# Kernel optimization log

Measured on AMD Instinct MI355X. Metric: run time of the kernel, lower is better.

The kernel has to match this reference:

```python
import jax, jax.numpy as jnp
import numpy as np

B, N, E, D, H, OUT = 4, 20000, 320000, 64, 128, 64
EPS = 1e-5


def layernorm(x, g, b):
    m = x.mean(-1, keepdims=True)
    v = x.var(-1, keepdims=True)
    return (x - m) / jnp.sqrt(v + EPS) * g + b


def setup_inputs() -> dict:
    key = jax.random.key(0)
    ks = jax.random.split(key, 20)
    nodes = jax.random.normal(ks[0], (B, N, D), jnp.float32)
    edges = jax.random.randint(ks[1], (B, E, 2), 0, N)
    edge_weights = jax.random.uniform(ks[2], (B, E), dtype=jnp.float32)
    s = 0.05
    inp = {"nodes": nodes, "edges": edges, "edge_weights": edge_weights}
    dims = [(3 * D, H), (H, H), (H, H), (H, OUT)]
    for i, (di, do) in enumerate(dims, start=1):
        inp[f"W{i}"] = jax.random.normal(ks[2 + 4 * i], (di, do), jnp.float32) * s
        inp[f"b{i}"] = jax.random.normal(ks[3 + 4 * i], (do,), jnp.float32) * s
        inp[f"g{i}"] = 1.0 + jax.random.normal(ks[4 + 4 * i], (do,), jnp.float32) * s
        inp[f"t{i}"] = jax.random.normal(ks[5 + 4 * i], (do,), jnp.float32) * s
    return inp


def reference(nodes, edges, edge_weights,
              W1, b1, g1, t1, W2, b2, g2, t2,
              W3, b3, g3, t3, W4, b4, g4, t4):
    # gather source/dest node features per edge: [B, E, D]
    src_idx = edges[..., 0]  # [B, E]
    dst_idx = edges[..., 1]  # [B, E]
    w = edge_weights[..., None]  # [B, E, 1]
    in_feat = jnp.take_along_axis(nodes, src_idx[..., None], axis=1) * w
    out_feat = jnp.take_along_axis(nodes, dst_idx[..., None], axis=1) * w

    # scatter-sum per node (segment sum over flattened batch*node ids)
    off = jnp.arange(B, dtype=dst_idx.dtype)[:, None] * N
    agg_in = jax.ops.segment_sum(in_feat.reshape(B * E, D),
                                 (dst_idx + off).reshape(-1),
                                 num_segments=B * N).reshape(B, N, D)
    agg_out = jax.ops.segment_sum(out_feat.reshape(B * E, D),
                                  (src_idx + off).reshape(-1),
                                  num_segments=B * N).reshape(B, N, D)

    x = jnp.concatenate([agg_in, agg_out, nodes], axis=2)  # [B, N, 3D]
    x = jnp.tanh(layernorm(x @ W1 + b1, g1, t1))
    x = jnp.tanh(layernorm(x @ W2 + b2, g2, t2))
    x = jnp.tanh(layernorm(x @ W3 + b3, g3, t3))
    x = jnp.tanh(layernorm(x @ W4 + b4, g4, t4))
    return x
```

## Files before the change

### kernel.cpp

```cpp
#include <hip/hip_runtime.h>
#include <math.h>

constexpr int Bc   = 4;
constexpr int Nc   = 20000;
constexpr int Ec   = 320000;
constexpr int Dc   = 64;
constexpr int ROWS = Bc * Nc;
constexpr int NSL  = 79;
constexpr int NBK  = 2 * Bc * NSL;
constexpr int CAP  = 48;
constexpr int EPW  = 2560;
constexpr int WPB  = 125;
constexpr int NWG  = Bc * WPB;
constexpr int TPW  = 128;
#define EPS 1e-5f

typedef __attribute__((ext_vector_type(8))) _Float16 f16x8;
typedef __attribute__((ext_vector_type(4))) float f32x4;

constexpr int CH32  = 5120;
constexpr int CH4c  = 2560;
constexpr int WQ_L2 = 30720;
constexpr int WQ_L3 = 51200;
constexpr int WQ_L4 = 71680;
constexpr int WQ_TOT = 81920;

__global__ __launch_bounds__(256) void conv_nodes(
    const float* __restrict__ nodes, _Float16* __restrict__ n16) {
    int i = (blockIdx.x * 256 + threadIdx.x) * 8;
    float4 a = *(const float4*)(nodes + i);
    float4 b = *(const float4*)(nodes + i + 4);
    f16x8 h;
    h[0] = (_Float16)a.x; h[1] = (_Float16)a.y; h[2] = (_Float16)a.z; h[3] = (_Float16)a.w;
    h[4] = (_Float16)b.x; h[5] = (_Float16)b.y; h[6] = (_Float16)b.z; h[7] = (_Float16)b.w;
    *(f16x8*)(n16 + i) = h;
}

__global__ __launch_bounds__(256) void local_bin(
    const int2* __restrict__ edges, const float* __restrict__ ew,
    uint2* __restrict__ staging, int* __restrict__ tblS, int* __restrict__ tblC) {
    __shared__ int cnt[256];
    __shared__ int offs[256];
    __shared__ int wsum[4];
    __shared__ uint2 stg[EPW * 2];

    const int tid = threadIdx.x;
    const int wg  = blockIdx.x;
    const int b   = wg / WPB;
    const int wgl = wg - b * WPB;
    const int base = wg * EPW;
    const int lane = tid & 63, wid = tid >> 6;

    cnt[tid] = 0;
    __syncthreads();

    int2 e[10]; unsigned wb[10];
#pragma unroll
    for (int j = 0; j < 10; ++j) {
        int idx = base + j * 256 + tid;
        e[j]  = edges[idx];
        wb[j] = __float_as_uint(ew[idx]);
    }

#pragma unroll
    for (int j = 0; j < 10; ++j) {
        atomicAdd(&cnt[e[j].y >> 8], 1);
        atomicAdd(&cnt[79 + (e[j].x >> 8)], 1);
    }
    __syncthreads();

    int v = cnt[tid];
    int incl = v;
#pragma unroll
    for (int d = 1; d < 64; d <<= 1) {
        int t = __shfl_up(incl, d, 64);
        if (lane >= d) incl += t;
    }
    if (lane == 63) wsum[wid] = incl;
    __syncthreads();
    int add = 0;
#pragma unroll
    for (int w = 0; w < 4; ++w)
        if (w < wid) add += wsum[w];
    offs[tid] = incl - v + add;
    __syncthreads();

    if (tid < 158) {
        int lb = tid;
        int row = (lb < 79) ? (b * NSL + lb) : (Bc * NSL + b * NSL + (lb - 79));
        tblS[row * TPW + wgl] = offs[lb];
        tblC[row * TPW + wgl] = cnt[lb];
    }
    __syncthreads();

#pragma unroll
    for (int j = 0; j < 10; ++j) {
        int pA = atomicAdd(&offs[e[j].y >> 8], 1);
        stg[pA] = make_uint2(((unsigned)(e[j].y & 255) << 16) | (unsigned)e[j].x, wb[j]);
        int pB = atomicAdd(&offs[79 + (e[j].x >> 8)], 1);
        stg[pB] = make_uint2(((unsigned)(e[j].x & 255) << 16) | (unsigned)e[j].y, wb[j]);
    }
    __syncthreads();

    uint2* outp = staging + (size_t)wg * (EPW * 2);
#pragma unroll
    for (int it = 0; it < 20; ++it)
        outp[it * 256 + tid] = stg[it * 256 + tid];
}

__global__ __launch_bounds__(512) void sort_bins(
    const uint2* __restrict__ staging,
    const int* __restrict__ tblS, const int* __restrict__ tblC,
    unsigned* __restrict__ list, int* __restrict__ cnt) {
    __shared__ unsigned lds[256 * CAP];
    __shared__ int lcnt[256];
    __shared__ int segS[WPB], segC[WPB];

    const int tid    = threadIdx.x;
    const int bucket = blockIdx.x;
    const int lane   = tid & 63, wid = tid >> 6;

    const int dir   = bucket >= Bc * NSL;
    const int rem   = bucket - dir * Bc * NSL;
    const int b     = rem / NSL;
    const int slice = rem % NSL;
    const int node0 = slice << 8;

    for (int i = tid; i < 256 * CAP; i += 512) lds[i] = 0u;
    if (tid < 256) lcnt[tid] = 0;
    if (tid < WPB) {
        int st = tblS[bucket * TPW + tid];
        int c  = tblC[bucket * TPW + tid];
        if (st < 0) st = 0; if (st > EPW * 2) st = EPW * 2;
        if (c  < 0) c  = 0; if (c  > EPW * 2 - st) c = EPW * 2 - st;
        segS[tid] = st;
        segC[tid] = c;
    }
    __syncthreads();

    for (int s = wid; s < WPB; s += 8) {
        int c = segC[s];
        const uint2* sp = staging + (size_t)(b * WPB + s) * (EPW * 2) + segS[s];
        for (int l0 = 0; l0 < c; l0 += 64) {
            if (lane < c - l0) {
                uint2 en = sp[l0 + lane];
                int local = en.x >> 16;
                unsigned nbr  = en.x & 0xFFFFu;
                unsigned wtop = (en.y + 0x4000u) & 0xFFFF8000u;
                int p = atomicAdd(&lcnt[local], 1);
                if (p < CAP) lds[local * CAP + p] = wtop | nbr;
            }
        }
    }
    __syncthreads();

    int nvalid = Nc - node0; if (nvalid > 256) nvalid = 256;
    const int keybase = dir * ROWS + b * Nc + node0;

    if (tid < nvalid) {
        int vv = lcnt[tid];
        cnt[keybase + tid] = vv < CAP ? vv : CAP;
    }
    unsigned* outp = list + (size_t)keybase * CAP;
    const int total = nvalid * CAP;
    for (int i = tid; i < total; i += 512)
        outp[i] = lds[i];
}

__global__ __launch_bounds__(256) void gather_kernel(
    const _Float16* __restrict__ n16,
    const unsigned* __restrict__ list,
    const int* __restrict__ cnt,
    _Float16* __restrict__ agg16_in, _Float16* __restrict__ agg16_out) {
    const int wid  = __builtin_amdgcn_readfirstlane(threadIdx.x >> 6);
    const int lane = threadIdx.x & 63;
    const int bid  = blockIdx.x;
    const int xcd  = bid & 7;
    const int loc  = bid >> 3;
    const int key  = xcd * 20000 + loc * 4 + wid;
    const int dir  = key >= ROWS;
    const int bn   = key - dir * ROWS;
    const int b    = bn / Nc;
    const _Float16* nb = n16 + (size_t)b * Nc * Dc;

    const int c = cnt[key];
    const unsigned* lp = list + (size_t)key * CAP;
    float acc0 = 0.f, acc1 = 0.f;
    for (int i = 0; i < c; i += 16) {
        uint4 ea = *(const uint4*)(lp + i);
        uint4 eb = *(const uint4*)(lp + i + 4);
        uint4 ec = *(const uint4*)(lp + i + 8);
        uint4 ed = *(const uint4*)(lp + i + 12);
        unsigned ev[16] = {ea.x, ea.y, ea.z, ea.w, eb.x, eb.y, eb.z, eb.w,
                           ec.x, ec.y, ec.z, ec.w, ed.x, ed.y, ed.z, ed.w};
        unsigned se[16];
        float r[16];
#pragma unroll
        for (int j = 0; j < 16; ++j) {
            se[j] = __builtin_amdgcn_readfirstlane(ev[j]);
            const _Float16* rp = nb + ((size_t)(se[j] & 0x7FFFu) << 6);
            r[j] = (float)rp[lane];
        }
#pragma unroll
        for (int j = 0; j < 16; j += 2) {
            acc0 = fmaf(r[j],     __uint_as_float(se[j]     & 0xFFFF8000u), acc0);
            acc1 = fmaf(r[j + 1], __uint_as_float(se[j + 1] & 0xFFFF8000u), acc1);
        }
    }
    float acc = acc0 + acc1;
    _Float16* dst = dir ? agg16_out : agg16_in;
    dst[(size_t)bn * Dc + lane] = (_Float16)acc;
}

__device__ inline float fast_tanh(float x) {
    float e = exp2f(x * 2.885390081777927f);
    return 1.0f - 2.0f * __builtin_amdgcn_rcpf(e + 1.0f);
}

__global__ __launch_bounds__(256) void prep_w(
    const float* __restrict__ W1, const float* __restrict__ W2,
    const float* __restrict__ W3, const float* __restrict__ W4,
    _Float16* __restrict__ wp) {
    int idx = blockIdx.x * 256 + threadIdx.x;
    const float* W; int DOl, base;
    if (idx < WQ_L2)      { W = W1; DOl = 128; base = 0; }
    else if (idx < WQ_L3) { W = W2; DOl = 128; base = WQ_L2; }
    else if (idx < WQ_L4) { W = W3; DOl = 128; base = WQ_L3; }
    else                  { W = W4; DOl = 64;  base = WQ_L4; }
    int local = idx - base;
    int chsz = DOl * 40;
    int chunk = local / chsz, rem = local - chunk * chsz;
    int col = rem / 40, kk = rem - col * 40;
    int k = chunk * 32 + kk;
    float v = (kk < 32) ? W[(size_t)k * DOl + col] : 0.f;
    wp[idx] = (_Float16)v;
}

__global__ __launch_bounds__(256, 4) void mlp_fused(
    const _Float16* __restrict__ agg16_in,
    const _Float16* __restrict__ agg16_out,
    const _Float16* __restrict__ n16,
    const _Float16* __restrict__ wp,
    const float* __restrict__ b1, const float* __restrict__ g1, const float* __restrict__ t1,
    const float* __restrict__ b2, const float* __restrict__ g2, const float* __restrict__ t2,
    const float* __restrict__ b3, const float* __restrict__ g3, const float* __restrict__ t3,
    const float* __restrict__ b4, const float* __restrict__ g4, const float* __restrict__ t4,
    float* __restrict__ out) {
    constexpr int XS = 136;
    __shared__ __align__(16) _Float16 wbuf[2][CH32];
    __shared__ __align__(16) _Float16 xh[64 * XS];

    const int tid = threadIdx.x;
    const int wv  = tid >> 6;
    const int l   = tid & 63;
    const int lm  = l & 15;
    const int lg  = l >> 4;
    const int rowloc = wv * 16;
    const int arow = blockIdx.x * 64 + rowloc + lm;
    const int koff = lg * 8;

    uint4 s0_ = {}, s1_ = {}, s2_ = {};

#define STAGE_LOAD(OFFH, N4)                                                      \
    {                                                                             \
        const uint4* s_ = (const uint4*)(wp + (OFFH));                            \
        if (tid < (N4))       s0_ = s_[tid];                                      \
        if (tid + 256 < (N4)) s1_ = s_[tid + 256];                                \
        if (tid + 512 < (N4)) s2_ = s_[tid + 512];                                \
    }
#define STAGE_WRITE(BUFI, N4)                                                     \
    {                                                                             \
        uint4* d_ = (uint4*)wbuf[BUFI];                                           \
        if (tid < (N4))       d_[tid] = s0_;                                      \
        if (tid + 256 < (N4)) d_[tid + 256] = s1_;                                \
        if (tid + 512 < (N4)) d_[tid + 512] = s2_;                                \
    }

    f32x4 acc[8] = {};
#define ZERO_ACC                                                                  \
    {                                                                             \
        _Pragma("unroll")                                                         \
        for (int ct = 0; ct < 8; ++ct) acc[ct] = (f32x4){0.f, 0.f, 0.f, 0.f};     \
    }

#define L1_COMPUTE(BUFI, SRC16, SUBK)                                             \
    {                                                                             \
        f16x8 ah = *(const f16x8*)((SRC16) + (size_t)arow * 64 + (SUBK) * 32 + koff); \
        _Pragma("unroll")                                                         \
        for (int ct = 0; ct < 8; ++ct) {                                          \
            int col = ct * 16 + lm;                                               \
            f16x8 bh = *(const f16x8*)(wbuf[BUFI] + col * 40 + koff);             \
            acc[ct] = __builtin_amdgcn_mfma_f32_16x16x32_f16(ah, bh, acc[ct], 0, 0, 0); \
        }                                                                         \
    }

#define LX_COMPUTE(BUFI, KIDX, NCTv)                                              \
    {                                                                             \
        f16x8 ah = *(const f16x8*)(xh + (rowloc + lm) * XS + (KIDX) * 32 + koff); \
        _Pragma("unroll")                                                         \
        for (int ct = 0; ct < NCTv; ++ct) {                                       \
            int col = ct * 16 + lm;                                               \
            f16x8 bh = *(const f16x8*)(wbuf[BUFI] + col * 40 + koff);             \
            acc[ct] = __builtin_amdgcn_mfma_f32_16x16x32_f16(ah, bh, acc[ct], 0, 0, 0); \
        }                                                                         \
    }

#define EPILOGUE(NCTv, DOv, BIAS, GG, TT, STORE_LDS)                              \
    {                                                                             \
        float s[4] = {0, 0, 0, 0}, ss[4] = {0, 0, 0, 0};                          \
        _Pragma("unroll")                                                         \
        for (int ct = 0; ct < NCTv; ++ct) {                                       \
            float bc = BIAS[ct * 16 + lm];                                        \
            _Pragma("unroll")                                                     \
            for (int r = 0; r < 4; ++r) {                                         \
                float v = acc[ct][r] + bc;                                        \
                acc[ct][r] = v;                                                   \
                s[r] += v; ss[r] += v * v;                                        \
            }                                                                     \
        }                                                                         \
        _Pragma("unroll")                                                         \
        for (int m = 1; m < 16; m <<= 1) {                                        \
            _Pragma("unroll")                                                     \
            for (int r = 0; r < 4; ++r) {                                         \
                s[r]  += __shfl_xor(s[r],  m, 64);                                \
                ss[r] += __shfl_xor(ss[r], m, 64);                                \
            }                                                                     \
        }                                                                         \
        float mean[4], rstd[4];                                                   \
        _Pragma("unroll")                                                         \
        for (int r = 0; r < 4; ++r) {                                             \
            mean[r] = s[r] * (1.0f / DOv);                                        \
            float var = ss[r] * (1.0f / DOv) - mean[r] * mean[r];                 \
            rstd[r] = rsqrtf(var + EPS);                                          \
        }                                                                         \
        _Pragma("unroll")                                                         \
        for (int ct = 0; ct < NCTv; ++ct) {                                       \
            int col = ct * 16 + lm;                                               \
            float gc = GG[col], tc = TT[col];                                     \
            _Pragma("unroll")                                                     \
            for (int r = 0; r < 4; ++r) {                                         \
                float v = (acc[ct][r] - mean[r]) * rstd[r] * gc + tc;             \
                float th = fast_tanh(v);                                          \
                int row = rowloc + lg * 4 + r;                                    \
                if (STORE_LDS) {                                                  \
                    xh[row * XS + col] = (_Float16)th;                            \
                } else {                                                          \
                    out[(size_t)(blockIdx.x * 64 + row) * 64 + col] = th;         \
                }                                                                 \
            }                                                                     \
        }                                                                         \
    }

    STAGE_LOAD(0, 640)
    STAGE_WRITE(0, 640)
    __syncthreads();

    STAGE_LOAD(CH32, 640)
    L1_COMPUTE(0, agg16_in, 0)
    STAGE_WRITE(1, 640)
    __syncthreads();

    STAGE_LOAD(2 * CH32, 640)
    L1_COMPUTE(1, agg16_in, 1)
    STAGE_WRITE(0, 640)
    __syncthreads();

    STAGE_LOAD(3 * CH32, 640)
    L1_COMPUTE(0, agg16_out, 0)
    STAGE_WRITE(1, 640)
    __syncthreads();

    STAGE_LOAD(4 * CH32, 640)
    L1_COMPUTE(1, agg16_out, 1)
    STAGE_WRITE(0, 640)
    __syncthreads();

    STAGE_LOAD(5 * CH32, 640)
    L1_COMPUTE(0, n16, 0)
    STAGE_WRITE(1, 640)
    __syncthreads();

    STAGE_LOAD(WQ_L2, 640)
    L1_COMPUTE(1, n16, 1)
    EPILOGUE(8, 128, b1, g1, t1, 1)
    STAGE_WRITE(0, 640)
    __syncthreads();
    ZERO_ACC

    STAGE_LOAD(WQ_L2 + CH32, 640)
    LX_COMPUTE(0, 0, 8)
    STAGE_WRITE(1, 640)
    __syncthreads();

    STAGE_LOAD(WQ_L2 + 2 * CH32, 640)
    LX_COMPUTE(1, 1, 8)
    STAGE_WRITE(0, 640)
    __syncthreads();

    STAGE_LOAD(WQ_L2 + 3 * CH32, 640)
    LX_COMPUTE(0, 2, 8)
    STAGE_WRITE(1, 640)
    __syncthreads();

    STAGE_LOAD(WQ_L3, 640)
    LX_COMPUTE(1, 3, 8)
    EPILOGUE(8, 128, b2, g2, t2, 1)
    STAGE_WRITE(0, 640)
    __syncthreads();
    ZERO_ACC

    STAGE_LOAD(WQ_L3 + CH32, 640)
    LX_COMPUTE(0, 0, 8)
    STAGE_WRITE(1, 640)
    __syncthreads();

    STAGE_LOAD(WQ_L3 + 2 * CH32, 640)
    LX_COMPUTE(1, 1, 8)
    STAGE_WRITE(0, 640)
    __syncthreads();

    STAGE_LOAD(WQ_L3 + 3 * CH32, 640)
    LX_COMPUTE(0, 2, 8)
    STAGE_WRITE(1, 640)
    __syncthreads();

    STAGE_LOAD(WQ_L4, 320)
    LX_COMPUTE(1, 3, 8)
    EPILOGUE(8, 128, b3, g3, t3, 1)
    STAGE_WRITE(0, 320)
    __syncthreads();
    ZERO_ACC

    STAGE_LOAD(WQ_L4 + CH4c, 320)
    LX_COMPUTE(0, 0, 4)
    STAGE_WRITE(1, 320)
    __syncthreads();

    STAGE_LOAD(WQ_L4 + 2 * CH4c, 320)
    LX_COMPUTE(1, 1, 4)
    STAGE_WRITE(0, 320)
    __syncthreads();

    STAGE_LOAD(WQ_L4 + 3 * CH4c, 320)
    LX_COMPUTE(0, 2, 4)
    STAGE_WRITE(1, 320)
    __syncthreads();

    LX_COMPUTE(1, 3, 4)
    EPILOGUE(4, 64, b4, g4, t4, 0)

#undef STAGE_LOAD
#undef STAGE_WRITE
#undef ZERO_ACC
#undef L1_COMPUTE
#undef LX_COMPUTE
#undef EPILOGUE
}

extern "C" void kernel_launch(void* const* d_in, const int* in_sizes, int n_in,
                              void* d_out, int out_size, void* d_ws, size_t ws_size,
                              hipStream_t stream) {
    const float* nodes = (const float*)d_in[0];
    const int*   edges = (const int*)d_in[1];
    const float* ew    = (const float*)d_in[2];
    const float* W1 = (const float*)d_in[3];
    const float* b1 = (const float*)d_in[4];
    const float* g1 = (const float*)d_in[5];
    const float* t1 = (const float*)d_in[6];
    const float* W2 = (const float*)d_in[7];
    const float* b2 = (const float*)d_in[8];
    const float* g2 = (const float*)d_in[9];
    const float* t2 = (const float*)d_in[10];
    const float* W3 = (const float*)d_in[11];
    const float* b3 = (const float*)d_in[12];
    const float* g3 = (const float*)d_in[13];
    const float* t3 = (const float*)d_in[14];
    const float* W4 = (const float*)d_in[15];
    const float* b4 = (const float*)d_in[16];
    const float* g4 = (const float*)d_in[17];
    const float* t4 = (const float*)d_in[18];

    float* out = (float*)d_out;

    const size_t AGG = (size_t)ROWS * Dc;
    float* ws      = (float*)d_ws;

    uint2*    staging = (uint2*)ws;
    _Float16* agg16_in  = (_Float16*)ws;
    _Float16* agg16_out = (_Float16*)(ws + AGG / 2);
    int*      tblS    = (int*)(ws + AGG);
    int*      tblC    = (int*)(ws + AGG) + (size_t)NBK * TPW;
    _Float16* n16     = (_Float16*)(ws + AGG + 262144);
    unsigned* list    = (unsigned*)(ws + 2 * AGG);
    int*      cnt     = (int*)(ws + 2 * AGG + (size_t)ROWS * 2 * CAP);

    _Float16* wp = (_Float16*)(ws + 4 * AGG);

    const int2* e2 = (const int2*)edges;

    prep_w<<<WQ_TOT / 256, 256, 0, stream>>>(W1, W2, W3, W4, wp);
    conv_nodes<<<(int)(AGG / 2048), 256, 0, stream>>>(nodes, n16);

    local_bin<<<NWG, 256, 0, stream>>>(e2, ew, staging, tblS, tblC);
    sort_bins<<<NBK, 512, 0, stream>>>(staging, tblS, tblC, list, cnt);

    gather_kernel<<<2 * ROWS / 4, 256, 0, stream>>>(n16, list, cnt,
                                                    agg16_in, agg16_out);

    mlp_fused<<<ROWS / 64, 256, 0, stream>>>(
        agg16_in, agg16_out, n16, wp,
        b1, g1, t1, b2, g2, t2, b3, g3, t3, b4, g4, t4, out);
}
```

Baseline: 123.0 us.

## Double MLP row tile per block and interleave two segments in bin sort

The fused MLP kernel now gives each wave 32 rows (two 16-row MFMA fragments) instead of 16, so every weight fragment loaded from LDS feeds two MFMAs. Each block now covers 128 rows and the weight staging is shared across twice as many rows. The cost is a larger accumulator set, so launch bounds drop to 2 blocks per CU and the grid is halved. Separately, the sort_bins kernel has each wave issue loads for two staging segments before doing their LDS atomics, to overlap global load latency.

```diff
diff --git a/kernel.cpp b/kernel.cpp
--- a/kernel.cpp
+++ b/kernel.cpp
@@ -138,20 +138,34 @@
     }
     __syncthreads();
 
-    for (int s = wid; s < WPB; s += 8) {
-        int c = segC[s];
-        const uint2* sp = staging + (size_t)(b * WPB + s) * (EPW * 2) + segS[s];
-        for (int l0 = 0; l0 < c; l0 += 64) {
-            if (lane < c - l0) {
-                uint2 en = sp[l0 + lane];
-                int local = en.x >> 16;
-                unsigned nbr  = en.x & 0xFFFFu;
-                unsigned wtop = (en.y + 0x4000u) & 0xFFFF8000u;
-                int p = atomicAdd(&lcnt[local], 1);
-                if (p < CAP) lds[local * CAP + p] = wtop | nbr;
-            }
-        }
-    }
+#define INSERT(EN)                                                                \
+    {                                                                             \
+        int local = (EN).x >> 16;                                                 \
+        unsigned nbr  = (EN).x & 0xFFFFu;                                         \
+        unsigned wtop = ((EN).y + 0x4000u) & 0xFFFF8000u;                         \
+        int p = atomicAdd(&lcnt[local], 1);                                       \
+        if (p < CAP) lds[local * CAP + p] = wtop | nbr;                           \
+    }
+
+    for (int s = wid; s < WPB; s += 16) {
+        const int s1 = s + 8;
+        const int c0 = segC[s];
+        const int c1 = (s1 < WPB) ? segC[s1] : 0;
+        const uint2* sp0 = staging + (size_t)(b * WPB + s) * (EPW * 2) + segS[s];
+        const uint2* sp1 = (s1 < WPB)
+            ? staging + (size_t)(b * WPB + s1) * (EPW * 2) + segS[s1] : sp0;
+        uint2 e0, e1;
+        const bool v0 = lane < c0, v1 = lane < c1;
+        if (v0) e0 = sp0[lane];
+        if (v1) e1 = sp1[lane];
+        if (v0) INSERT(e0)
+        if (v1) INSERT(e1)
+        for (int l0 = 64; l0 < c0; l0 += 64)
+            if (lane < c0 - l0) { uint2 e = sp0[l0 + lane]; INSERT(e) }
+        for (int l0 = 64; l0 < c1; l0 += 64)
+            if (lane < c1 - l0) { uint2 e = sp1[l0 + lane]; INSERT(e) }
+    }
+#undef INSERT
     __syncthreads();
 
     int nvalid = Nc - node0; if (nvalid > 256) nvalid = 256;
@@ -236,7 +250,7 @@
     wp[idx] = (_Float16)v;
 }
 
-__global__ __launch_bounds__(256, 4) void mlp_fused(
+__global__ __launch_bounds__(256, 2) void mlp_fused(
     const _Float16* __restrict__ agg16_in,
     const _Float16* __restrict__ agg16_out,
     const _Float16* __restrict__ n16,
@@ -248,15 +262,15 @@
     float* __restrict__ out) {
     constexpr int XS = 136;
     __shared__ __align__(16) _Float16 wbuf[2][CH32];
-    __shared__ __align__(16) _Float16 xh[64 * XS];
+    __shared__ __align__(16) _Float16 xh[128 * XS];
 
     const int tid = threadIdx.x;
     const int wv  = tid >> 6;
     const int l   = tid & 63;
     const int lm  = l & 15;
     const int lg  = l >> 4;
-    const int rowloc = wv * 16;
-    const int arow = blockIdx.x * 64 + rowloc + lm;
+    const int rowloc = wv * 32;
+    const int arow = blockIdx.x * 128 + rowloc + lm;
     const int koff = lg * 8;
 
     uint4 s0_ = {}, s1_ = {}, s2_ = {};
@@ -276,76 +290,83 @@
         if (tid + 512 < (N4)) d_[tid + 512] = s2_;                                \
     }
 
-    f32x4 acc[8] = {};
+    f32x4 acc[16] = {};
 #define ZERO_ACC                                                                  \
     {                                                                             \
         _Pragma("unroll")                                                         \
-        for (int ct = 0; ct < 8; ++ct) acc[ct] = (f32x4){0.f, 0.f, 0.f, 0.f};     \
+        for (int q = 0; q < 16; ++q) acc[q] = (f32x4){0.f, 0.f, 0.f, 0.f};        \
     }
 
 #define L1_COMPUTE(BUFI, SRC16, SUBK)                                             \
     {                                                                             \
-        f16x8 ah = *(const f16x8*)((SRC16) + (size_t)arow * 64 + (SUBK) * 32 + koff); \
+        f16x8 ah0 = *(const f16x8*)((SRC16) + (size_t)arow * 64 + (SUBK) * 32 + koff);       \
+        f16x8 ah1 = *(const f16x8*)((SRC16) + (size_t)(arow + 16) * 64 + (SUBK) * 32 + koff);\
         _Pragma("unroll")                                                         \
         for (int ct = 0; ct < 8; ++ct) {                                          \
             int col = ct * 16 + lm;                                               \
             f16x8 bh = *(const f16x8*)(wbuf[BUFI] + col * 40 + koff);             \
-            acc[ct] = __builtin_amdgcn_mfma_f32_16x16x32_f16(ah, bh, acc[ct], 0, 0, 0); \
+            acc[ct]     = __builtin_amdgcn_mfma_f32_16x16x32_f16(ah0, bh, acc[ct], 0, 0, 0);     \
+            acc[8 + ct] = __builtin_amdgcn_mfma_f32_16x16x32_f16(ah1, bh, acc[8 + ct], 0, 0, 0); \
         }                                                                         \
     }
 
 #define LX_COMPUTE(BUFI, KIDX, NCTv)                                              \
     {                                                                             \
-        f16x8 ah = *(const f16x8*)(xh + (rowloc + lm) * XS + (KIDX) * 32 + koff); \
+        f16x8 ah0 = *(const f16x8*)(xh + (rowloc + lm) * XS + (KIDX) * 32 + koff);      \
+        f16x8 ah1 = *(const f16x8*)(xh + (rowloc + 16 + lm) * XS + (KIDX) * 32 + koff); \
         _Pragma("unroll")                                                         \
         for (int ct = 0; ct < NCTv; ++ct) {                                       \
             int col = ct * 16 + lm;                                               \
             f16x8 bh = *(const f16x8*)(wbuf[BUFI] + col * 40 + koff);             \
-            acc[ct] = __builtin_amdgcn_mfma_f32_16x16x32_f16(ah, bh, acc[ct], 0, 0, 0); \
+            acc[ct]     = __builtin_amdgcn_mfma_f32_16x16x32_f16(ah0, bh, acc[ct], 0, 0, 0);     \
+            acc[8 + ct] = __builtin_amdgcn_mfma_f32_16x16x32_f16(ah1, bh, acc[8 + ct], 0, 0, 0); \
         }                                                                         \
     }
 
 #define EPILOGUE(NCTv, DOv, BIAS, GG, TT, STORE_LDS)                              \
     {                                                                             \
-        float s[4] = {0, 0, 0, 0}, ss[4] = {0, 0, 0, 0};                          \
         _Pragma("unroll")                                                         \
-        for (int ct = 0; ct < NCTv; ++ct) {                                       \
-            float bc = BIAS[ct * 16 + lm];                                        \
+        for (int rf = 0; rf < 2; ++rf) {                                          \
+            float s[4] = {0, 0, 0, 0}, ss[4] = {0, 0, 0, 0};                      \
+            _Pragma("unroll")                                                     \
+            for (int ct = 0; ct < NCTv; ++ct) {                                   \
+                float bc = BIAS[ct * 16 + lm];                                    \
+                _Pragma("unroll")                                                 \
+                for (int r = 0; r < 4; ++r) {                                     \
+                    float v = acc[rf * 8 + ct][r] + bc;                           \
+                    acc[rf * 8 + ct][r] = v;                                      \
+                    s[r] += v; ss[r] += v * v;                                    \
+                }                                                                 \
+            }                                                                     \
+            _Pragma("unroll")                                                     \
+            for (int m = 1; m < 16; m <<= 1) {                                    \
+                _Pragma("unroll")                                                 \
+                for (int r = 0; r < 4; ++r) {                                     \
+                    s[r]  += __shfl_xor(s[r],  m, 64);                            \
+                    ss[r] += __shfl_xor(ss[r], m, 64);                            \
+                }                                                                 \
+            }                                                                     \
+            float mean[4], rstd[4];                                               \
             _Pragma("unroll")                                                     \
             for (int r = 0; r < 4; ++r) {                                         \
-                float v = acc[ct][r] + bc;                                        \
-                acc[ct][r] = v;                                                   \
-                s[r] += v; ss[r] += v * v;                                        \
+                mean[r] = s[r] * (1.0f / DOv);                                    \
+                float var = ss[r] * (1.0f / DOv) - mean[r] * mean[r];             \
+                rstd[r] = rsqrtf(var + EPS);                                      \
             }                                                                     \
-        }                                                                         \
-        _Pragma("unroll")                                                         \
-        for (int m = 1; m < 16; m <<= 1) {                                        \
             _Pragma("unroll")                                                     \
-            for (int r = 0; r < 4; ++r) {                                         \
-                s[r]  += __shfl_xor(s[r],  m, 64);                                \
-                ss[r] += __shfl_xor(ss[r], m, 64);                                \
-            }                                                                     \
-        }                                                                         \
-        float mean[4], rstd[4];                                                   \
-        _Pragma("unroll")                                                         \
-        for (int r = 0; r < 4; ++r) {                                             \
-            mean[r] = s[r] * (1.0f / DOv);                                        \
-            float var = ss[r] * (1.0f / DOv) - mean[r] * mean[r];                 \
-            rstd[r] = rsqrtf(var + EPS);                                          \
-        }                                                                         \
-        _Pragma("unroll")                                                         \
-        for (int ct = 0; ct < NCTv; ++ct) {                                       \
-            int col = ct * 16 + lm;                                               \
-            float gc = GG[col], tc = TT[col];                                     \
-            _Pragma("unroll")                                                     \
-            for (int r = 0; r < 4; ++r) {                                         \
-                float v = (acc[ct][r] - mean[r]) * rstd[r] * gc + tc;             \
-                float th = fast_tanh(v);                                          \
-                int row = rowloc + lg * 4 + r;                                    \
-                if (STORE_LDS) {                                                  \
-                    xh[row * XS + col] = (_Float16)th;                            \
-                } else {                                                          \
-                    out[(size_t)(blockIdx.x * 64 + row) * 64 + col] = th;         \
+            for (int ct = 0; ct < NCTv; ++ct) {                                   \
+                int col = ct * 16 + lm;                                           \
+                float gc = GG[col], tc = TT[col];                                 \
+                _Pragma("unroll")                                                 \
+                for (int r = 0; r < 4; ++r) {                                     \
+                    float v = (acc[rf * 8 + ct][r] - mean[r]) * rstd[r] * gc + tc;\
+                    float th = fast_tanh(v);                                      \
+                    int row = rowloc + rf * 16 + lg * 4 + r;                      \
+                    if (STORE_LDS) {                                              \
+                        xh[row * XS + col] = (_Float16)th;                        \
+                    } else {                                                      \
+                        out[(size_t)(blockIdx.x * 128 + row) * 64 + col] = th;    \
+                    }                                                             \
                 }                                                                 \
             }                                                                     \
         }                                                                         \
@@ -507,7 +528,7 @@
     gather_kernel<<<2 * ROWS / 4, 256, 0, stream>>>(n16, list, cnt,
                                                     agg16_in, agg16_out);
 
-    mlp_fused<<<ROWS / 64, 256, 0, stream>>>(
+    mlp_fused<<<ROWS / 128, 256, 0, stream>>>(
         agg16_in, agg16_out, n16, wp,
         b1, g1, t1, b2, g2, t2, b3, g3, t3, b4, g4, t4, out);
 }
```

After: 131.3 us. 6.7% more time.
